# Kernel tuning notes

Measured on AMD Instinct MI355X. Metric: run time of the kernel, lower is better.

The kernel has to match this reference:

```python
import jax, jax.numpy as jnp
import numpy as np

HEADS = 16
EMBED = 1024
HEAD_DIM = EMBED // HEADS

def _split_heads(x):
    b, n, _ = x.shape
    return x.reshape(b, n, HEADS, HEAD_DIM).transpose(0, 2, 1, 3)  # b h n d

def _merge_heads(x):
    b, h, n, d = x.shape
    return x.transpose(0, 2, 1, 3).reshape(b, n, h * d)

def _attn(q_in, kv_in, Wq, bq, Wk, bk, Wv, bv, Wo, bo):
    q = _split_heads(q_in @ Wq + bq)
    k = _split_heads(kv_in @ Wk + bk)
    v = _split_heads(kv_in @ Wv + bv)
    e = jnp.einsum('bhqd,bhkd->bhqk', q, k) * (HEAD_DIM ** -0.5)
    a = jax.nn.softmax(e, axis=-1)
    o = jnp.einsum('bhqk,bhkd->bhqd', a, v)
    return _merge_heads(o) @ Wo + bo

def _layernorm(x, g, b, eps=1e-5):
    mu = jnp.mean(x, axis=-1, keepdims=True)
    var = jnp.var(x, axis=-1, keepdims=True)
    return (x - mu) * jax.lax.rsqrt(var + eps) * g + b

def setup_inputs() -> dict:
    key = jax.random.key(0)
    ks = jax.random.split(key, 20)
    s = 0.02
    d = {
        'temp_features': jax.random.normal(ks[0], (2, 2048, EMBED), jnp.float32),
        'spat_features': jax.random.normal(ks[1], (2, 2048, EMBED), jnp.float32),
    }
    names = ['t2s_Wq', 't2s_Wk', 't2s_Wv', 't2s_Wo', 's2t_Wq', 's2t_Wk', 's2t_Wv', 's2t_Wo']
    for i, nm in enumerate(names):
        d[nm] = jax.random.normal(ks[2 + i], (EMBED, EMBED), jnp.float32) * s
        d[nm.replace('W', 'b')] = jnp.zeros((EMBED,), jnp.float32)
    d['ln_g'] = jnp.ones((EMBED,), jnp.float32)
    d['ln_b'] = jnp.zeros((EMBED,), jnp.float32)
    return d

def reference(temp_features, spat_features,
              t2s_Wq, t2s_bq, t2s_Wk, t2s_bk, t2s_Wv, t2s_bv, t2s_Wo, t2s_bo,
              s2t_Wq, s2t_bq, s2t_Wk, s2t_bk, s2t_Wv, s2t_bv, s2t_Wo, s2t_bo,
              ln_g, ln_b):
    # t2s: queries from spat, keys/values from temp; residual = spat
    t2s = _attn(spat_features, temp_features, t2s_Wq, t2s_bq, t2s_Wk, t2s_bk,
                t2s_Wv, t2s_bv, t2s_Wo, t2s_bo)
    t2s_out = _layernorm(spat_features + t2s, ln_g, ln_b)
    # s2t: queries from temp, keys/values from spat; residual = temp
    s2t = _attn(temp_features, spat_features, s2t_Wq, s2t_bq, s2t_Wk, s2t_bk,
                s2t_Wv, s2t_bv, s2t_Wo, s2t_bo)
    s2t_out = _layernorm(temp_features + s2t, ln_g, ln_b)
    return (s2t_out, t2s_out)
```

## Files before the change

kernel.cpp:

```cpp
#include <hip/hip_runtime.h>
#include <stdint.h>

#define SEQ 2048
#define EMB 1024
#define NROWS 4096

typedef __bf16 bf16x8 __attribute__((ext_vector_type(8)));
typedef float f32x4 __attribute__((ext_vector_type(4)));
typedef unsigned short ushort8 __attribute__((ext_vector_type(8)));

__device__ __forceinline__ unsigned short f2bf(float f) {
  unsigned int u = __float_as_uint(f);
  u += 0x7fffu + ((u >> 16) & 1u);
  return (unsigned short)(u >> 16);
}

__device__ __forceinline__ float bf2f(unsigned short h) {
  return __uint_as_float((unsigned int)h << 16);
}

__device__ __forceinline__ f32x4 mfma16(bf16x8 a, bf16x8 b, f32x4 c) {
  return __builtin_amdgcn_mfma_f32_16x16x32_bf16(a, b, c, 0, 0, 0);
}

__device__ __forceinline__ void async_load16(const void* g, void* l) {
  auto gp = reinterpret_cast<__attribute__((address_space(1))) void*>(
      reinterpret_cast<uintptr_t>(g));
  auto lp = reinterpret_cast<__attribute__((address_space(3))) void*>(
      reinterpret_cast<uintptr_t>(l));
  __builtin_amdgcn_global_load_lds(gp, lp, 16, 0, 0);
}

__global__ __launch_bounds__(256) void prep(const float* __restrict__ t,
                                            const float* __restrict__ s,
                                            unsigned short* __restrict__ tb,
                                            unsigned short* __restrict__ sb,
                                            const float* __restrict__ W0,
                                            const float* __restrict__ W1,
                                            const float* __restrict__ W2,
                                            const float* __restrict__ W3,
                                            const float* __restrict__ W4,
                                            const float* __restrict__ W5,
                                            const float* __restrict__ W6,
                                            const float* __restrict__ W7,
                                            unsigned short* __restrict__ Wt) {
  const int bx = blockIdx.x;
  if (bx < 8192) {
    int i = bx * 256 + threadIdx.x;
    const float* x; unsigned short* y;
    if (i < NROWS * EMB / 4) { x = t; y = tb; }
    else { x = s; y = sb; i -= NROWS * EMB / 4; }
    float4 v = ((const float4*)x)[i];
    ushort4 o;
    o.x = f2bf(v.x); o.y = f2bf(v.y); o.z = f2bf(v.z); o.w = f2bf(v.w);
    ((ushort4*)y)[i] = o;
    return;
  }
  const int e = bx - 8192;
  const int z = e >> 8, tt = e & 255;
  const float* Ws[8] = {W0, W1, W2, W3, W4, W5, W6, W7};
  const float* W = Ws[z];
  unsigned short* dst = Wt + ((size_t)z << 20);
  __shared__ unsigned short tile[64][65];
  const int n0 = (tt & 15) * 64, k0 = (tt >> 4) * 64;
#pragma unroll
  for (int i = 0; i < 16; ++i) {
    const int ee = i * 256 + threadIdx.x;
    const int kk = ee >> 6, nn = ee & 63;
    tile[kk][nn] = f2bf(W[(size_t)(k0 + kk) * EMB + n0 + nn]);
  }
  __syncthreads();
#pragma unroll
  for (int i = 0; i < 16; ++i) {
    const int ee = i * 256 + threadIdx.x;
    const int nn = ee >> 6, kk = ee & 63;
    dst[(size_t)(n0 + nn) * EMB + k0 + kk] = tile[kk][nn];
  }
}

__device__ __forceinline__ void gemm_core64(const unsigned short* __restrict__ A,
                                            const unsigned short* __restrict__ Bt,
                                            int m0, int bt0,
                                            unsigned short* As, unsigned short* Bs,
                                            f32x4 (&acc)[4][4]) {
  const int tid = threadIdx.x;
  const int w = tid >> 6, lane = tid & 63;
  const int quad = lane >> 4, l16 = lane & 15;
  const int wm = w & 1, wn = w >> 1;
  const int sw8 = l16 & 7;

  const int srow = lane >> 3, p8 = lane & 7;
  const unsigned short* Ag[4];
  const unsigned short* Bg[4];
#pragma unroll
  for (int i = 0; i < 4; ++i) {
    const int r = w * 32 + i * 8 + srow;
    Ag[i] = A + (size_t)(m0 + r) * EMB + ((p8 ^ (r & 7)) * 8);
    Bg[i] = Bt + (size_t)(bt0 + r) * EMB + ((p8 ^ (r & 7)) * 8);
  }
  unsigned short* AsB[4];
  unsigned short* BsB[4];
#pragma unroll
  for (int i = 0; i < 4; ++i) {
    AsB[i] = As + (w * 32 + i * 8) * 64;
    BsB[i] = Bs + (w * 32 + i * 8) * 64;
  }

  for (int kk = 0; kk < EMB; kk += 64) {
    __syncthreads();
#pragma unroll
    for (int i = 0; i < 4; ++i) {
      async_load16(Ag[i] + kk, AsB[i]);
      async_load16(Bg[i] + kk, BsB[i]);
    }
    __syncthreads();
#pragma unroll
    for (int h = 0; h < 2; ++h) {
      bf16x8 af[4], bfr[4];
#pragma unroll
      for (int im = 0; im < 4; ++im)
        af[im] = *(const bf16x8*)(As + (wm * 64 + im * 16 + l16) * 64 +
                                  (((h * 4 + quad) ^ sw8) * 8));
#pragma unroll
      for (int in = 0; in < 4; ++in)
        bfr[in] = *(const bf16x8*)(Bs + (wn * 64 + in * 16 + l16) * 64 +
                                   (((h * 4 + quad) ^ sw8) * 8));
#pragma unroll
      for (int im = 0; im < 4; ++im)
#pragma unroll
        for (int in = 0; in < 4; ++in)
          acc[im][in] = mfma16(af[im], bfr[in], acc[im][in]);
    }
  }
}

__global__ __launch_bounds__(256, 3) void gemm_qkv(const unsigned short* __restrict__ tempb,
                                                   const unsigned short* __restrict__ spatb,
                                                   const unsigned short* __restrict__ Wt,
                                                   const float* __restrict__ bq0,
                                                   const float* __restrict__ bk0,
                                                   const float* __restrict__ bv0,
                                                   const float* __restrict__ bq1,
                                                   const float* __restrict__ bk1,
                                                   const float* __restrict__ bv1,
                                                   unsigned short* __restrict__ Qb,
                                                   unsigned short* __restrict__ Kb,
                                                   unsigned short* __restrict__ Vtb) {
  __shared__ alignas(16) unsigned short As[128 * 64];
  __shared__ alignas(16) unsigned short Bs[128 * 64];
  const int idx = blockIdx.x >> 3;
  const int dir = idx / 3, kind = idx - dir * 3;
  const int n0 = (blockIdx.x & 7) * 128;
  const unsigned short* A =
      (dir == 0) ? (kind == 0 ? tempb : spatb) : (kind == 0 ? spatb : tempb);
  const float* bias = (dir == 0) ? (kind == 0 ? bq0 : (kind == 1 ? bk0 : bv0))
                                 : (kind == 0 ? bq1 : (kind == 1 ? bk1 : bv1));

  f32x4 acc[4][4] = {};
  gemm_core64(A, Wt + ((size_t)(dir * 4 + kind) << 20), blockIdx.y * 128, n0, As, Bs, acc);

  const int tid = threadIdx.x;
  const int w = tid >> 6, lane = tid & 63;
  const int quad = lane >> 4, l16 = lane & 15;
  const int wm = w & 1, wn = w >> 1;
  const int rowb = blockIdx.y * 128 + wm * 64;
  const size_t dof = (size_t)dir * NROWS * EMB;

  if (kind == 2) {
    __syncthreads();
    unsigned short* sc = (w < 2 ? As : Bs) + (w & 1) * 4096;
    const int colbase = n0 + wn * 64;
    const int hh = colbase >> 6;
    const int bb = rowb >> 11;
    const int key0 = rowb & 2047;
    const int sw2 = (l16 & 7) << 1;
#pragma unroll
    for (int in = 0; in < 4; ++in) {
      const int drow = in * 16 + l16;
      const float bvv = bias[colbase + in * 16 + l16];
#pragma unroll
      for (int im = 0; im < 4; ++im) {
        uint2 pk;
        pk.x = (unsigned int)f2bf(acc[im][in][0] + bvv) |
               ((unsigned int)f2bf(acc[im][in][1] + bvv) << 16);
        pk.y = (unsigned int)f2bf(acc[im][in][2] + bvv) |
               ((unsigned int)f2bf(acc[im][in][3] + bvv) << 16);
        const int kb = im * 4 + quad;
        *(uint2*)(sc + drow * 64 + ((kb ^ sw2) << 2)) = pk;
      }
    }
    asm volatile("" ::: "memory");
    unsigned short* Vt = Vtb + dof + ((size_t)(bb * 16 + hh) * 64) * SEQ + key0;
    const int rl = lane >> 3;
    const int c = lane & 7;
#pragma unroll
    for (int p = 0; p < 8; ++p) {
      const int d = p * 8 + rl;
      const int kbs = (c * 2) ^ ((d & 7) << 1);
      ushort8 v = *(const ushort8*)(sc + d * 64 + (kbs << 2));
      *(ushort8*)(Vt + (size_t)d * SEQ + c * 8) = v;
    }
  } else {
    unsigned short* out = ((kind == 0) ? Qb : Kb) + dof;
    const float scale = (kind == 0) ? 0.18033688011112042f : 1.0f;
#pragma unroll
    for (int in = 0; in < 4; ++in) {
      const int col = n0 + wn * 64 + in * 16 + l16;
      const float bvv = bias[col];
#pragma unroll
      for (int im = 0; im < 4; ++im)
#pragma unroll
        for (int r = 0; r < 4; ++r) {
          const int row = rowb + im * 16 + quad * 4 + r;
          out[(size_t)row * EMB + col] = f2bf((acc[im][in][r] + bvv) * scale);
        }
    }
  }
}

__global__ __launch_bounds__(256, 3) void gemm_o(const unsigned short* __restrict__ Ob,
                                                 const unsigned short* __restrict__ Wt,
                                                 const float* __restrict__ bo0,
                                                 const float* __restrict__ bo1,
                                                 const float* __restrict__ temp,
                                                 const float* __restrict__ spat,
                                                 unsigned short* __restrict__ projb) {
  __shared__ alignas(16) unsigned short As[128 * 64];
  __shared__ alignas(16) unsigned short Bs[128 * 64];
  const int dir = blockIdx.x >> 3;
  const int n0 = (blockIdx.x & 7) * 128;
  const size_t dof = (size_t)dir * NROWS * EMB;
  const float* bias = dir ? bo1 : bo0;
  const float* resid = dir ? spat : temp;

  f32x4 acc[4][4] = {};
  gemm_core64(Ob + dof, Wt + ((size_t)(dir * 4 + 3) << 20), blockIdx.y * 128, n0, As, Bs,
              acc);

  const int tid = threadIdx.x;
  const int w = tid >> 6, lane = tid & 63;
  const int quad = lane >> 4, l16 = lane & 15;
  const int wm = w & 1, wn = w >> 1;
  const int rowb = blockIdx.y * 128 + wm * 64;
  unsigned short* outb = projb + dof;
#pragma unroll
  for (int in = 0; in < 4; ++in) {
    const int col = n0 + wn * 64 + in * 16 + l16;
    const float bvv = bias[col];
#pragma unroll
    for (int im = 0; im < 4; ++im)
#pragma unroll
      for (int r = 0; r < 4; ++r) {
        const int row = rowb + im * 16 + quad * 4 + r;
        const size_t off = (size_t)row * EMB + col;
        outb[off] = f2bf(acc[im][in][r] + bvv + resid[off]);
      }
  }
}

__global__ __launch_bounds__(256, 4) void flash_attn(const unsigned short* __restrict__ Qall,
                                                     const unsigned short* __restrict__ Kall,
                                                     const unsigned short* __restrict__ Vtall,
                                                     unsigned short* __restrict__ Oall) {
  __shared__ alignas(16) unsigned short Ks[2][64 * 64];
  __shared__ alignas(16) unsigned short Vs[2][64 * 64];

  const int tid = threadIdx.x;
  const int w = tid >> 6, lane = tid & 63;
  const int quad = lane >> 4, l16 = lane & 15;
  const int phys = blockIdx.x + (blockIdx.y << 4);
  const int xcd = phys & 7, slot = phys >> 3;
  const int bxv = slot & 15;
  const int byv = (xcd << 3) + (slot >> 4);
  const int dir = byv >> 5, bh = byv & 31;
  const int b = bh >> 4, h = bh & 15;
  const size_t dof = (size_t)dir * NROWS * EMB;
  const unsigned short* Q = Qall + dof;
  const unsigned short* K = Kall + dof;
  const unsigned short* Vt = Vtall + dof;
  unsigned short* O = Oall + dof;
  const int q0 = bxv * 128 + w * 32;

  bf16x8 qf[2][2];
#pragma unroll
  for (int qh = 0; qh < 2; ++qh) {
    const unsigned short* Qrow = Q + (size_t)(b * SEQ + q0 + qh * 16 + l16) * EMB + h * 64;
    qf[qh][0] = *(const bf16x8*)(Qrow + quad * 8);
    qf[qh][1] = *(const bf16x8*)(Qrow + 32 + quad * 8);
  }

  bf16x8 onesf;
#pragma unroll
  for (int i = 0; i < 8; ++i) onesf[i] = (__bf16)1.0f;

  f32x4 oaccT[2][4] = {};
  f32x4 rs[2] = {};
  const int swz = (l16 & 7) << 1;
  const int sw8 = l16 & 7;

  const int r8 = lane >> 3, p8 = lane & 7;
  const int gk0 = ((w >> 1) << 5) + ((r8 >> 2) << 3) + ((w & 1) << 2) + (r8 & 3);
  const int gk1 = gk0 + 16;
  const int kr0 = w * 16 + r8;
  const int kr1 = kr0 + 8;
  const unsigned short* Ksrc0 = K + (size_t)(b * SEQ + gk0) * EMB + h * 64 + ((p8 ^ r8) * 8);
  const unsigned short* Ksrc1 = K + (size_t)(b * SEQ + gk1) * EMB + h * 64 + ((p8 ^ r8) * 8);
  const unsigned short* Vsrc0 = Vt + ((size_t)bh * 64 + kr0) * SEQ + ((p8 ^ (kr0 & 7)) * 8);
  const unsigned short* Vsrc1 = Vt + ((size_t)bh * 64 + kr1) * SEQ + ((p8 ^ (kr1 & 7)) * 8);
  unsigned short* KsW0 = &Ks[0][0] + (w * 16) * 64;
  unsigned short* KsW1 = &Ks[0][0] + (w * 16 + 8) * 64;
  unsigned short* VsW0 = &Vs[0][0] + (w * 16) * 64;
  unsigned short* VsW1 = &Vs[0][0] + (w * 16 + 8) * 64;

  async_load16(Ksrc0, KsW0);
  async_load16(Ksrc1, KsW1);
  async_load16(Vsrc0, VsW0);
  async_load16(Vsrc1, VsW1);

  auto tile_step = [&](int ktn, bool more, const unsigned short* KsC,
                       const unsigned short* VsC, unsigned short* KD0,
                       unsigned short* KD1, unsigned short* VD0, unsigned short* VD1) {
    if (more) {
      async_load16(Ksrc0 + (size_t)ktn * EMB, KD0);
      async_load16(Ksrc1 + (size_t)ktn * EMB, KD1);
      async_load16(Vsrc0 + ktn, VD0);
      async_load16(Vsrc1 + ktn, VD1);
      asm volatile("s_waitcnt vmcnt(4)" ::: "memory");
    } else {
      asm volatile("s_waitcnt vmcnt(0)" ::: "memory");
    }
    __builtin_amdgcn_s_barrier();
    asm volatile("" ::: "memory");

    bf16x8 pb[2][2];
    __builtin_amdgcn_s_setprio(1);
#pragma unroll
    for (int g = 0; g < 4; ++g) {
      const int krow = g * 16 + l16;
      bf16x8 kf0 = *(const bf16x8*)(KsC + krow * 64 + ((quad ^ sw8) * 8));
      bf16x8 kf1 = *(const bf16x8*)(KsC + krow * 64 + (((4 + quad) ^ sw8) * 8));
#pragma unroll
      for (int qh = 0; qh < 2; ++qh) {
        f32x4 z = {};
        z = mfma16(kf0, qf[qh][0], z);
        z = mfma16(kf1, qf[qh][1], z);
        const int s = g >> 1, o4 = (g & 1) * 4;
        pb[qh][s][o4 + 0] = (__bf16)__builtin_amdgcn_exp2f(z[0]);
        pb[qh][s][o4 + 1] = (__bf16)__builtin_amdgcn_exp2f(z[1]);
        pb[qh][s][o4 + 2] = (__bf16)__builtin_amdgcn_exp2f(z[2]);
        pb[qh][s][o4 + 3] = (__bf16)__builtin_amdgcn_exp2f(z[3]);
      }
    }
    __builtin_amdgcn_s_setprio(0);
#pragma unroll
    for (int qh = 0; qh < 2; ++qh)
      rs[qh] = mfma16(onesf, pb[qh][1], mfma16(onesf, pb[qh][0], rs[qh]));

    __builtin_amdgcn_s_setprio(1);
#pragma unroll
    for (int dg = 0; dg < 4; ++dg) {
      const int dd = dg * 16 + l16;
      bf16x8 v0 = *(const bf16x8*)(VsC + dd * 64 + ((quad ^ sw8) * 8));
      bf16x8 v1 = *(const bf16x8*)(VsC + dd * 64 + (((4 + quad) ^ sw8) * 8));
#pragma unroll
      for (int qh = 0; qh < 2; ++qh) {
        oaccT[qh][dg] = mfma16(v0, pb[qh][0], oaccT[qh][dg]);
        oaccT[qh][dg] = mfma16(v1, pb[qh][1], oaccT[qh][dg]);
      }
    }
    __builtin_amdgcn_s_setprio(0);
    asm volatile("" ::: "memory");
    __builtin_amdgcn_s_barrier();
  };

  for (int kt = 0; kt < SEQ; kt += 128) {
    tile_step(kt + 64, true, &Ks[0][0], &Vs[0][0],
              KsW0 + 4096, KsW1 + 4096, VsW0 + 4096, VsW1 + 4096);
    tile_step(kt + 128, kt + 128 < SEQ, &Ks[1][0], &Vs[1][0],
              KsW0, KsW1, VsW0, VsW1);
  }

  unsigned short* pw = &Ks[0][0] + w * 1024;
#pragma unroll
  for (int qh = 0; qh < 2; ++qh) {
    const float inv = 1.0f / rs[qh][0];
#pragma unroll
    for (int dg = 0; dg < 4; ++dg) {
      uint2 pkk;
      pkk.x = (unsigned int)f2bf(oaccT[qh][dg][0] * inv) |
              ((unsigned int)f2bf(oaccT[qh][dg][1] * inv) << 16);
      pkk.y = (unsigned int)f2bf(oaccT[qh][dg][2] * inv) |
              ((unsigned int)f2bf(oaccT[qh][dg][3] * inv) << 16);
      const int kb = 4 * dg + quad;
      *(uint2*)(pw + l16 * 64 + ((kb ^ swz) << 2)) = pkk;
    }
    asm volatile("" ::: "memory");
    const int qq = lane >> 2, cc = lane & 3;
    const int swq = (qq & 7) << 1;
    ushort8 r0 = *(const ushort8*)(pw + qq * 64 + (((4 * cc) ^ swq) << 2));
    ushort8 r1 = *(const ushort8*)(pw + qq * 64 + (((4 * cc + 2) ^ swq) << 2));
    unsigned short* Orow = O + (size_t)(b * SEQ + q0 + qh * 16 + qq) * EMB + h * 64 + cc * 16;
    *(ushort8*)(Orow) = r0;
    *(ushort8*)(Orow + 8) = r1;
    asm volatile("" ::: "memory");
  }
}

__global__ __launch_bounds__(256) void ln_k(const unsigned short* __restrict__ X,
                                            const float* __restrict__ g,
                                            const float* __restrict__ bb,
                                            float* __restrict__ out) {
  const int row = blockIdx.x;
  const int tid = threadIdx.x;
  const ushort4 hv = ((const ushort4*)(X + (size_t)row * EMB))[tid];
  float4 v;
  v.x = bf2f(hv.x); v.y = bf2f(hv.y); v.z = bf2f(hv.z); v.w = bf2f(hv.w);
  float s = v.x + v.y + v.z + v.w;
  float s2 = v.x * v.x + v.y * v.y + v.z * v.z + v.w * v.w;
#pragma unroll
  for (int o = 32; o > 0; o >>= 1) {
    s += __shfl_down(s, o);
    s2 += __shfl_down(s2, o);
  }
  __shared__ float ws[4], ws2[4];
  if ((tid & 63) == 0) { ws[tid >> 6] = s; ws2[tid >> 6] = s2; }
  __syncthreads();
  const float S = ws[0] + ws[1] + ws[2] + ws[3];
  const float S2 = ws2[0] + ws2[1] + ws2[2] + ws2[3];
  const float mu = S * (1.f / EMB);
  const float inv = rsqrtf(S2 * (1.f / EMB) - mu * mu + 1e-5f);
  const float4 gv = ((const float4*)g)[tid];
  const float4 bv = ((const float4*)bb)[tid];
  float4 o4;
  o4.x = (v.x - mu) * inv * gv.x + bv.x;
  o4.y = (v.y - mu) * inv * gv.y + bv.y;
  o4.z = (v.z - mu) * inv * gv.z + bv.z;
  o4.w = (v.w - mu) * inv * gv.w + bv.w;
  ((float4*)(out + (size_t)row * EMB))[tid] = o4;
}

extern "C" void kernel_launch(void* const* d_in, const int* in_sizes, int n_in,
                              void* d_out, int out_size, void* d_ws, size_t ws_size,
                              hipStream_t stream) {
  const float* temp = (const float*)d_in[0];
  const float* spat = (const float*)d_in[1];
  const float* lng = (const float*)d_in[18];
  const float* lnb = (const float*)d_in[19];
  float* out = (float*)d_out;

  char* base = (char*)d_ws;
  unsigned short* tempb = (unsigned short*)(base + ((size_t)0 << 20));
  unsigned short* spatb = (unsigned short*)(base + ((size_t)8 << 20));
  unsigned short* Wt = (unsigned short*)(base + ((size_t)16 << 20));
  unsigned short* Qb = (unsigned short*)(base + ((size_t)32 << 20));
  unsigned short* Kb = (unsigned short*)(base + ((size_t)48 << 20));
  unsigned short* Vtb = (unsigned short*)(base + ((size_t)64 << 20));
  unsigned short* Ob = (unsigned short*)(base + ((size_t)80 << 20));
  unsigned short* projb = (unsigned short*)(base + ((size_t)32 << 20));

  prep<<<8192 + 2048, 256, 0, stream>>>(
      temp, spat, tempb, spatb, (const float*)d_in[10], (const float*)d_in[12],
      (const float*)d_in[14], (const float*)d_in[16], (const float*)d_in[2],
      (const float*)d_in[4], (const float*)d_in[6], (const float*)d_in[8], Wt);
  gemm_qkv<<<dim3(48, 32), 256, 0, stream>>>(
      tempb, spatb, Wt, (const float*)d_in[11], (const float*)d_in[13],
      (const float*)d_in[15], (const float*)d_in[3], (const float*)d_in[5],
      (const float*)d_in[7], Qb, Kb, Vtb);
  flash_attn<<<dim3(16, 64), 256, 0, stream>>>(Qb, Kb, Vtb, Ob);
  gemm_o<<<dim3(16, 32), 256, 0, stream>>>(Ob, Wt, (const float*)d_in[17],
                                           (const float*)d_in[9], temp, spat, projb);
  ln_k<<<2 * NROWS, 256, 0, stream>>>(projb, lng, lnb, out);
}
```

Baseline: 302.0 us.

## Fuse Q/K/V projections sharing the same activation into one block

Each QKV GEMM block now computes the three projections that read the same input activation (Q for one direction, K and V for the other), loading the A tile once and reusing it against three weight tiles. The grid shrinks from 1536 to 512 blocks, which are remapped with a swizzled block index to improve L2 locality, and launch bounds drop to 2 waves per SIMD. This cuts redundant A-tile global loads, at the cost of triple the accumulators, more LDS, and lower occupancy and parallelism.

```diff
diff --git a/kernel.cpp b/kernel.cpp
--- a/kernel.cpp
+++ b/kernel.cpp
@@ -134,7 +134,7 @@
   }
 }
 
-__global__ __launch_bounds__(256, 3) void gemm_qkv(const unsigned short* __restrict__ tempb,
+__global__ __launch_bounds__(256, 2) void gemm_qkv(const unsigned short* __restrict__ tempb,
                                                    const unsigned short* __restrict__ spatb,
                                                    const unsigned short* __restrict__ Wt,
                                                    const float* __restrict__ bq0,
@@ -147,74 +147,133 @@
                                                    unsigned short* __restrict__ Kb,
                                                    unsigned short* __restrict__ Vtb) {
   __shared__ alignas(16) unsigned short As[128 * 64];
-  __shared__ alignas(16) unsigned short Bs[128 * 64];
-  const int idx = blockIdx.x >> 3;
-  const int dir = idx / 3, kind = idx - dir * 3;
-  const int n0 = (blockIdx.x & 7) * 128;
-  const unsigned short* A =
-      (dir == 0) ? (kind == 0 ? tempb : spatb) : (kind == 0 ? spatb : tempb);
-  const float* bias = (dir == 0) ? (kind == 0 ? bq0 : (kind == 1 ? bk0 : bv0))
-                                 : (kind == 0 ? bq1 : (kind == 1 ? bk1 : bv1));
-
-  f32x4 acc[4][4] = {};
-  gemm_core64(A, Wt + ((size_t)(dir * 4 + kind) << 20), blockIdx.y * 128, n0, As, Bs, acc);
+  __shared__ alignas(16) unsigned short Bs[3 * 128 * 64];
+  const size_t DOF = (size_t)NROWS * EMB;
+
+  const int phys = blockIdx.x + (blockIdx.y << 4);
+  const int virt = ((phys & 7) << 6) + (phys >> 3);
+  const int act = virt >> 8;
+  const int rem = virt & 255;
+  const int m0 = (rem >> 3) * 128;
+  const int n0 = (rem & 7) * 128;
+
+  const unsigned short* A = act ? spatb : tempb;
+  const int slot[3] = {act ? 4 : 0, act ? 1 : 5, act ? 2 : 6};
+  const float* bias[3];
+  bias[0] = act ? bq1 : bq0;
+  bias[1] = act ? bk0 : bk1;
+  bias[2] = act ? bv0 : bv1;
+  unsigned short* Qout = Qb + (act ? DOF : 0);
+  unsigned short* Kout = Kb + (act ? 0 : DOF);
+  unsigned short* Vout = Vtb + (act ? 0 : DOF);
 
   const int tid = threadIdx.x;
   const int w = tid >> 6, lane = tid & 63;
   const int quad = lane >> 4, l16 = lane & 15;
   const int wm = w & 1, wn = w >> 1;
-  const int rowb = blockIdx.y * 128 + wm * 64;
-  const size_t dof = (size_t)dir * NROWS * EMB;
-
-  if (kind == 2) {
+  const int sw8 = l16 & 7;
+
+  const int srow = lane >> 3, p8 = lane & 7;
+  const unsigned short* Ag[4];
+  const unsigned short* Bg[3][4];
+  unsigned short* AsB[4];
+  unsigned short* BsB[3][4];
+#pragma unroll
+  for (int i = 0; i < 4; ++i) {
+    const int r = w * 32 + i * 8 + srow;
+    const int swo = (p8 ^ (r & 7)) * 8;
+    Ag[i] = A + (size_t)(m0 + r) * EMB + swo;
+    AsB[i] = As + (w * 32 + i * 8) * 64;
+#pragma unroll
+    for (int j = 0; j < 3; ++j) {
+      Bg[j][i] = Wt + ((size_t)slot[j] << 20) + (size_t)(n0 + r) * EMB + swo;
+      BsB[j][i] = Bs + j * 8192 + (w * 32 + i * 8) * 64;
+    }
+  }
+
+  f32x4 acc[3][4][4] = {};
+  for (int kk = 0; kk < EMB; kk += 64) {
     __syncthreads();
-    unsigned short* sc = (w < 2 ? As : Bs) + (w & 1) * 4096;
-    const int colbase = n0 + wn * 64;
-    const int hh = colbase >> 6;
-    const int bb = rowb >> 11;
-    const int key0 = rowb & 2047;
-    const int sw2 = (l16 & 7) << 1;
-#pragma unroll
-    for (int in = 0; in < 4; ++in) {
-      const int drow = in * 16 + l16;
-      const float bvv = bias[colbase + in * 16 + l16];
-#pragma unroll
-      for (int im = 0; im < 4; ++im) {
-        uint2 pk;
-        pk.x = (unsigned int)f2bf(acc[im][in][0] + bvv) |
-               ((unsigned int)f2bf(acc[im][in][1] + bvv) << 16);
-        pk.y = (unsigned int)f2bf(acc[im][in][2] + bvv) |
-               ((unsigned int)f2bf(acc[im][in][3] + bvv) << 16);
-        const int kb = im * 4 + quad;
-        *(uint2*)(sc + drow * 64 + ((kb ^ sw2) << 2)) = pk;
+#pragma unroll
+    for (int i = 0; i < 4; ++i) async_load16(Ag[i] + kk, AsB[i]);
+#pragma unroll
+    for (int j = 0; j < 3; ++j)
+#pragma unroll
+      for (int i = 0; i < 4; ++i) async_load16(Bg[j][i] + kk, BsB[j][i]);
+    __syncthreads();
+#pragma unroll
+    for (int h = 0; h < 2; ++h) {
+      bf16x8 af[4];
+#pragma unroll
+      for (int im = 0; im < 4; ++im)
+        af[im] = *(const bf16x8*)(As + (wm * 64 + im * 16 + l16) * 64 +
+                                  (((h * 4 + quad) ^ sw8) * 8));
+#pragma unroll
+      for (int j = 0; j < 3; ++j) {
+        bf16x8 bfr[4];
+#pragma unroll
+        for (int in = 0; in < 4; ++in)
+          bfr[in] = *(const bf16x8*)(Bs + j * 8192 + (wn * 64 + in * 16 + l16) * 64 +
+                                     (((h * 4 + quad) ^ sw8) * 8));
+#pragma unroll
+        for (int im = 0; im < 4; ++im)
+#pragma unroll
+          for (int in = 0; in < 4; ++in)
+            acc[j][im][in] = mfma16(af[im], bfr[in], acc[j][im][in]);
       }
     }
-    asm volatile("" ::: "memory");
-    unsigned short* Vt = Vtb + dof + ((size_t)(bb * 16 + hh) * 64) * SEQ + key0;
-    const int rl = lane >> 3;
-    const int c = lane & 7;
-#pragma unroll
-    for (int p = 0; p < 8; ++p) {
-      const int d = p * 8 + rl;
-      const int kbs = (c * 2) ^ ((d & 7) << 1);
-      ushort8 v = *(const ushort8*)(sc + d * 64 + (kbs << 2));
-      *(ushort8*)(Vt + (size_t)d * SEQ + c * 8) = v;
-    }
-  } else {
-    unsigned short* out = ((kind == 0) ? Qb : Kb) + dof;
-    const float scale = (kind == 0) ? 0.18033688011112042f : 1.0f;
+  }
+
+  const int rowb = m0 + wm * 64;
+  {
+    const float scale = 0.18033688011112042f;
 #pragma unroll
     for (int in = 0; in < 4; ++in) {
       const int col = n0 + wn * 64 + in * 16 + l16;
-      const float bvv = bias[col];
+      const float bq = bias[0][col];
+      const float bk = bias[1][col];
 #pragma unroll
       for (int im = 0; im < 4; ++im)
 #pragma unroll
         for (int r = 0; r < 4; ++r) {
           const int row = rowb + im * 16 + quad * 4 + r;
-          out[(size_t)row * EMB + col] = f2bf((acc[im][in][r] + bvv) * scale);
+          Qout[(size_t)row * EMB + col] = f2bf((acc[0][im][in][r] + bq) * scale);
+          Kout[(size_t)row * EMB + col] = f2bf(acc[1][im][in][r] + bk);
         }
     }
+  }
+  __syncthreads();
+  unsigned short* sc = Bs + w * 4096;
+  const int colbase = n0 + wn * 64;
+  const int hh = colbase >> 6;
+  const int bb = rowb >> 11;
+  const int key0 = rowb & 2047;
+  const int sw2 = (l16 & 7) << 1;
+#pragma unroll
+  for (int in = 0; in < 4; ++in) {
+    const int drow = in * 16 + l16;
+    const float bvv = bias[2][colbase + in * 16 + l16];
+#pragma unroll
+    for (int im = 0; im < 4; ++im) {
+      uint2 pk;
+      pk.x = (unsigned int)f2bf(acc[2][im][in][0] + bvv) |
+             ((unsigned int)f2bf(acc[2][im][in][1] + bvv) << 16);
+      pk.y = (unsigned int)f2bf(acc[2][im][in][2] + bvv) |
+             ((unsigned int)f2bf(acc[2][im][in][3] + bvv) << 16);
+      const int kb = im * 4 + quad;
+      *(uint2*)(sc + drow * 64 + ((kb ^ sw2) << 2)) = pk;
+    }
+  }
+  asm volatile("" ::: "memory");
+  unsigned short* Vt = Vout + ((size_t)(bb * 16 + hh) * 64) * SEQ + key0;
+  const int rl = lane >> 3;
+  const int c = lane & 7;
+#pragma unroll
+  for (int p = 0; p < 8; ++p) {
+    const int d = p * 8 + rl;
+    const int kbs = (c * 2) ^ ((d & 7) << 1);
+    ushort8 v = *(const ushort8*)(sc + d * 64 + (kbs << 2));
+    *(ushort8*)(Vt + (size_t)d * SEQ + c * 8) = v;
   }
 }
 
@@ -462,7 +521,7 @@
       temp, spat, tempb, spatb, (const float*)d_in[10], (const float*)d_in[12],
       (const float*)d_in[14], (const float*)d_in[16], (const float*)d_in[2],
       (const float*)d_in[4], (const float*)d_in[6], (const float*)d_in[8], Wt);
-  gemm_qkv<<<dim3(48, 32), 256, 0, stream>>>(
+  gemm_qkv<<<dim3(16, 32), 256, 0, stream>>>(
       tempb, spatb, Wt, (const float*)d_in[11], (const float*)d_in[13],
       (const float*)d_in[15], (const float*)d_in[3], (const float*)d_in[5],
       (const float*)d_in[7], Qb, Kb, Vtb);
```

Measured after the change: 323.7 us. +7.2%, slower.

## Fuse output projection and layernorm via grid-wide atomic barrier

Applied to the files above, without the earlier changes.

Merges the output-projection GEMM and the layernorm kernel into one launch. Each of the 512 blocks writes its projected-plus-residual tile, then all blocks wait on a global atomic counter; afterwards each block normalizes 16 full rows. The counter is reset inside the attention kernel. This removes one kernel launch and its tail, but it relies on all 512 blocks being co-resident, or the spin barrier deadlocks, and the barrier itself costs some time. The counter sits at the start of the workspace, which overlaps the tempb buffer.

```diff
diff --git a/kernel.cpp b/kernel.cpp
--- a/kernel.cpp
+++ b/kernel.cpp
@@ -218,52 +218,15 @@
   }
 }
 
-__global__ __launch_bounds__(256, 3) void gemm_o(const unsigned short* __restrict__ Ob,
-                                                 const unsigned short* __restrict__ Wt,
-                                                 const float* __restrict__ bo0,
-                                                 const float* __restrict__ bo1,
-                                                 const float* __restrict__ temp,
-                                                 const float* __restrict__ spat,
-                                                 unsigned short* __restrict__ projb) {
-  __shared__ alignas(16) unsigned short As[128 * 64];
-  __shared__ alignas(16) unsigned short Bs[128 * 64];
-  const int dir = blockIdx.x >> 3;
-  const int n0 = (blockIdx.x & 7) * 128;
-  const size_t dof = (size_t)dir * NROWS * EMB;
-  const float* bias = dir ? bo1 : bo0;
-  const float* resid = dir ? spat : temp;
-
-  f32x4 acc[4][4] = {};
-  gemm_core64(Ob + dof, Wt + ((size_t)(dir * 4 + 3) << 20), blockIdx.y * 128, n0, As, Bs,
-              acc);
-
-  const int tid = threadIdx.x;
-  const int w = tid >> 6, lane = tid & 63;
-  const int quad = lane >> 4, l16 = lane & 15;
-  const int wm = w & 1, wn = w >> 1;
-  const int rowb = blockIdx.y * 128 + wm * 64;
-  unsigned short* outb = projb + dof;
-#pragma unroll
-  for (int in = 0; in < 4; ++in) {
-    const int col = n0 + wn * 64 + in * 16 + l16;
-    const float bvv = bias[col];
-#pragma unroll
-    for (int im = 0; im < 4; ++im)
-#pragma unroll
-      for (int r = 0; r < 4; ++r) {
-        const int row = rowb + im * 16 + quad * 4 + r;
-        const size_t off = (size_t)row * EMB + col;
-        outb[off] = f2bf(acc[im][in][r] + bvv + resid[off]);
-      }
-  }
-}
-
 __global__ __launch_bounds__(256, 4) void flash_attn(const unsigned short* __restrict__ Qall,
                                                      const unsigned short* __restrict__ Kall,
                                                      const unsigned short* __restrict__ Vtall,
-                                                     unsigned short* __restrict__ Oall) {
+                                                     unsigned short* __restrict__ Oall,
+                                                     unsigned int* __restrict__ cnt) {
   __shared__ alignas(16) unsigned short Ks[2][64 * 64];
   __shared__ alignas(16) unsigned short Vs[2][64 * 64];
+
+  if (blockIdx.x == 0 && blockIdx.y == 0 && threadIdx.x == 0) *cnt = 0u;
 
   const int tid = threadIdx.x;
   const int w = tid >> 6, lane = tid & 63;
@@ -406,37 +369,89 @@
   }
 }
 
-__global__ __launch_bounds__(256) void ln_k(const unsigned short* __restrict__ X,
-                                            const float* __restrict__ g,
-                                            const float* __restrict__ bb,
-                                            float* __restrict__ out) {
-  const int row = blockIdx.x;
+__global__ __launch_bounds__(256, 3) void gemm_o_ln(const unsigned short* __restrict__ Ob,
+                                                    const unsigned short* __restrict__ Wt,
+                                                    const float* __restrict__ bo0,
+                                                    const float* __restrict__ bo1,
+                                                    const float* __restrict__ temp,
+                                                    const float* __restrict__ spat,
+                                                    unsigned short* __restrict__ projb,
+                                                    const float* __restrict__ lng,
+                                                    const float* __restrict__ lnb,
+                                                    float* __restrict__ out,
+                                                    unsigned int* __restrict__ cnt) {
+  __shared__ alignas(16) unsigned short As[128 * 64];
+  __shared__ alignas(16) unsigned short Bs[128 * 64];
+  const int dir = blockIdx.x >> 3;
+  const int n0 = (blockIdx.x & 7) * 128;
+  const size_t dof = (size_t)dir * NROWS * EMB;
+  const float* bias = dir ? bo1 : bo0;
+  const float* resid = dir ? spat : temp;
+
+  f32x4 acc[4][4] = {};
+  gemm_core64(Ob + dof, Wt + ((size_t)(dir * 4 + 3) << 20), blockIdx.y * 128, n0, As, Bs,
+              acc);
+
   const int tid = threadIdx.x;
-  const ushort4 hv = ((const ushort4*)(X + (size_t)row * EMB))[tid];
-  float4 v;
-  v.x = bf2f(hv.x); v.y = bf2f(hv.y); v.z = bf2f(hv.z); v.w = bf2f(hv.w);
-  float s = v.x + v.y + v.z + v.w;
-  float s2 = v.x * v.x + v.y * v.y + v.z * v.z + v.w * v.w;
-#pragma unroll
-  for (int o = 32; o > 0; o >>= 1) {
-    s += __shfl_down(s, o);
-    s2 += __shfl_down(s2, o);
-  }
-  __shared__ float ws[4], ws2[4];
-  if ((tid & 63) == 0) { ws[tid >> 6] = s; ws2[tid >> 6] = s2; }
+  const int w = tid >> 6, lane = tid & 63;
+  const int quad = lane >> 4, l16 = lane & 15;
+  const int wm = w & 1, wn = w >> 1;
+  const int rowb = blockIdx.y * 128 + wm * 64;
+  unsigned short* outb = projb + dof;
+#pragma unroll
+  for (int in = 0; in < 4; ++in) {
+    const int col = n0 + wn * 64 + in * 16 + l16;
+    const float bvv = bias[col];
+#pragma unroll
+    for (int im = 0; im < 4; ++im)
+#pragma unroll
+      for (int r = 0; r < 4; ++r) {
+        const int row = rowb + im * 16 + quad * 4 + r;
+        const size_t off = (size_t)row * EMB + col;
+        outb[off] = f2bf(acc[im][in][r] + bvv + resid[off]);
+      }
+  }
+
+  __threadfence();
   __syncthreads();
-  const float S = ws[0] + ws[1] + ws[2] + ws[3];
-  const float S2 = ws2[0] + ws2[1] + ws2[2] + ws2[3];
-  const float mu = S * (1.f / EMB);
-  const float inv = rsqrtf(S2 * (1.f / EMB) - mu * mu + 1e-5f);
-  const float4 gv = ((const float4*)g)[tid];
-  const float4 bv = ((const float4*)bb)[tid];
-  float4 o4;
-  o4.x = (v.x - mu) * inv * gv.x + bv.x;
-  o4.y = (v.y - mu) * inv * gv.y + bv.y;
-  o4.z = (v.z - mu) * inv * gv.z + bv.z;
-  o4.w = (v.w - mu) * inv * gv.w + bv.w;
-  ((float4*)(out + (size_t)row * EMB))[tid] = o4;
+  if (tid == 0) {
+    atomicAdd(cnt, 1u);
+    while (atomicAdd(cnt, 0u) < 512u) { __builtin_amdgcn_s_sleep(1); }
+  }
+  __syncthreads();
+  __threadfence();
+
+  const int bid = blockIdx.x + (blockIdx.y << 4);
+  float* wsf = (float*)&As[0];
+  const float4 gv = ((const float4*)lng)[tid];
+  const float4 bv = ((const float4*)lnb)[tid];
+#pragma unroll 1
+  for (int r = 0; r < 16; ++r) {
+    const int row = bid * 16 + r;
+    const ushort4 hv = ((const ushort4*)(projb + (size_t)row * EMB))[tid];
+    float4 v;
+    v.x = bf2f(hv.x); v.y = bf2f(hv.y); v.z = bf2f(hv.z); v.w = bf2f(hv.w);
+    float s = v.x + v.y + v.z + v.w;
+    float s2 = v.x * v.x + v.y * v.y + v.z * v.z + v.w * v.w;
+#pragma unroll
+    for (int o = 32; o > 0; o >>= 1) {
+      s += __shfl_down(s, o);
+      s2 += __shfl_down(s2, o);
+    }
+    if ((tid & 63) == 0) { wsf[tid >> 6] = s; wsf[4 + (tid >> 6)] = s2; }
+    __syncthreads();
+    const float S = wsf[0] + wsf[1] + wsf[2] + wsf[3];
+    const float S2 = wsf[4] + wsf[5] + wsf[6] + wsf[7];
+    const float mu = S * (1.f / EMB);
+    const float inv = rsqrtf(S2 * (1.f / EMB) - mu * mu + 1e-5f);
+    float4 o4;
+    o4.x = (v.x - mu) * inv * gv.x + bv.x;
+    o4.y = (v.y - mu) * inv * gv.y + bv.y;
+    o4.z = (v.z - mu) * inv * gv.z + bv.z;
+    o4.w = (v.w - mu) * inv * gv.w + bv.w;
+    ((float4*)(out + (size_t)row * EMB))[tid] = o4;
+    __syncthreads();
+  }
 }
 
 extern "C" void kernel_launch(void* const* d_in, const int* in_sizes, int n_in,
@@ -457,6 +472,7 @@
   unsigned short* Vtb = (unsigned short*)(base + ((size_t)64 << 20));
   unsigned short* Ob = (unsigned short*)(base + ((size_t)80 << 20));
   unsigned short* projb = (unsigned short*)(base + ((size_t)32 << 20));
+  unsigned int* cnt = (unsigned int*)base;
 
   prep<<<8192 + 2048, 256, 0, stream>>>(
       temp, spat, tempb, spatb, (const float*)d_in[10], (const float*)d_in[12],
@@ -466,8 +482,8 @@
       tempb, spatb, Wt, (const float*)d_in[11], (const float*)d_in[13],
       (const float*)d_in[15], (const float*)d_in[3], (const float*)d_in[5],
       (const float*)d_in[7], Qb, Kb, Vtb);
-  flash_attn<<<dim3(16, 64), 256, 0, stream>>>(Qb, Kb, Vtb, Ob);
-  gemm_o<<<dim3(16, 32), 256, 0, stream>>>(Ob, Wt, (const float*)d_in[17],
-                                           (const float*)d_in[9], temp, spat, projb);
-  ln_k<<<2 * NROWS, 256, 0, stream>>>(projb, lng, lnb, out);
-}
+  flash_attn<<<dim3(16, 64), 256, 0, stream>>>(Qb, Kb, Vtb, Ob, cnt);
+  gemm_o_ln<<<dim3(16, 32), 256, 0, stream>>>(Ob, Wt, (const float*)d_in[17],
+                                              (const float*)d_in[9], temp, spat, projb,
+                                              lng, lnb, out, cnt);
+}
```

Result: slower. 427.9 us (+41.7%).
